# Performance work log

Measured on AMD Instinct MI355X. Metric: run time of the kernel, lower is better.

## Reference

```python
import jax, jax.numpy as jnp
import numpy as np

N = 50000
E = 800000
F_IN = 500
ID_DIM = 128
HID = 128
N_CLS = 40


def _init_linear(key, fan_in, fan_out, bias=True):
    k1, k2 = jax.random.split(key)
    bound = 1.0 / np.sqrt(fan_in)
    W = jax.random.uniform(k1, (fan_in, fan_out), minval=-bound, maxval=bound, dtype=jnp.float32)
    if bias:
        b = jax.random.uniform(k2, (fan_out,), minval=-bound, maxval=bound, dtype=jnp.float32)
        return W, b
    return W, None


def setup_inputs() -> dict:
    key = jax.random.key(0)
    ks = jax.random.split(key, 10)
    x = jax.random.normal(ks[0], (N, F_IN), dtype=jnp.float32)
    edge_index = jax.random.randint(ks[1], (2, E), 0, N, dtype=jnp.int32)
    W_map, b_map = _init_linear(ks[2], F_IN, ID_DIM)
    Wl1, bl1 = _init_linear(ks[3], ID_DIM, HID)
    Wr1, _ = _init_linear(ks[4], ID_DIM, HID, bias=False)
    Wl2, bl2 = _init_linear(ks[5], HID, 2 * HID)
    Wr2, _ = _init_linear(ks[6], HID, 2 * HID, bias=False)
    Wl3, bl3 = _init_linear(ks[7], 2 * HID, N_CLS)
    Wr3, _ = _init_linear(ks[8], 2 * HID, N_CLS, bias=False)
    return {"x": x, "edge_index": edge_index,
            "W_map": W_map, "b_map": b_map,
            "Wl1": Wl1, "bl1": bl1, "Wr1": Wr1,
            "Wl2": Wl2, "bl2": bl2, "Wr2": Wr2,
            "Wl3": Wl3, "bl3": bl3, "Wr3": Wr3}


def _sage_conv(x, src, dst, Wl, bl, Wr):
    # mean aggregation of source features into destination nodes
    agg = jax.ops.segment_sum(x[src], dst, num_segments=N)  # [N, d]
    cnt = jax.ops.segment_sum(jnp.ones((src.shape[0],), x.dtype), dst, num_segments=N)
    mean = agg / jnp.maximum(cnt, 1.0)[:, None]
    # SAGEConv (normalize=False): lin_l(mean_neigh) + lin_r(x), bias only on lin_l
    return mean @ Wl + bl + x @ Wr


def reference(x, edge_index, W_map, b_map, Wl1, bl1, Wr1, Wl2, bl2, Wr2, Wl3, bl3, Wr3):
    src, dst = edge_index[0], edge_index[1]
    h = x @ W_map + b_map                      # [N, 128]
    h = jax.nn.relu(_sage_conv(h, src, dst, Wl1, bl1, Wr1))   # dropout is identity in eval
    h = jax.nn.relu(_sage_conv(h, src, dst, Wl2, bl2, Wr2))
    h = _sage_conv(h, src, dst, Wl3, bl3, Wr3)
    return jax.nn.log_softmax(h, axis=1)
```

## Files before the change

kernel.cpp:

```cpp
#include <hip/hip_runtime.h>
#include <math.h>

#define NN 50000
#define NE 800000
#define FIN 500
#define NCLS 40
#define NB 196

typedef short short8 __attribute__((ext_vector_type(8)));
typedef float f32x4 __attribute__((ext_vector_type(4)));

__device__ __forceinline__ unsigned short f2bf(float f) {
    unsigned u = __float_as_uint(f);
    unsigned r = (u + 0x7FFFu + ((u >> 16) & 1u)) >> 16;
    return (unsigned short)r;
}
__device__ __forceinline__ float bf2f(unsigned short h) {
    return __uint_as_float(((unsigned)h) << 16);
}

typedef const __attribute__((address_space(1))) void gv1;
typedef __attribute__((address_space(3))) void lv3;
__device__ __forceinline__ void gl16(const void* g, void* l) {
    __builtin_amdgcn_global_load_lds((gv1*)g, (lv3*)l, 16, 0, 0);
}

__global__ void k_wsplit(const float* __restrict__ W, short* __restrict__ dst,
                         int Ksrc, int Ncols, int Kpad, int BN, int koff,
                         int noff, int llog) {
    int i = blockIdx.x * 256 + threadIdx.x;
    int len = 1 << llog;
    if (i >= Ncols * len) return;
    int n = i >> llog, kk = i & (len - 1);
    float v = (kk < Ksrc) ? W[(size_t)kk * Ncols + n] : 0.f;
    unsigned short hi = f2bf(v);
    float lo = v - bf2f(hi);
    int nd = noff + n, kd = koff + kk;
    int yb = nd / BN, r = nd % BN;
    int ck = kd >> 6, kin = kd & 63;
    int c16h = (kin >> 3) ^ (r & 7);
    size_t rowb = (((size_t)yb * (Kpad >> 6) + ck) * BN + r) * 128;
    dst[rowb + c16h * 8 + (kin & 7)] = (short)hi;
    dst[rowb + (8 + c16h) * 8 + (kin & 7)] = (short)f2bf(lo);
}

__global__ void k_count(const int* __restrict__ dst, int* __restrict__ deg) {
    int e = blockIdx.x * blockDim.x + threadIdx.x;
    if (e < NE) atomicAdd(&deg[dst[e]], 1);
}

__global__ void k_scan1(const int* __restrict__ deg, int* __restrict__ offs,
                        int* __restrict__ bsum) {
    __shared__ int sm[256];
    int tid = threadIdx.x;
    int i = blockIdx.x * 256 + tid;
    int v = (i < NN) ? deg[i] : 0;
    sm[tid] = v;
    __syncthreads();
    for (int off = 1; off < 256; off <<= 1) {
        int t = (tid >= off) ? sm[tid - off] : 0;
        __syncthreads();
        sm[tid] += t;
        __syncthreads();
    }
    if (i < NN) offs[i] = sm[tid] - v;
    if (tid == 255) bsum[blockIdx.x] = sm[255];
}

__global__ void k_scan2(const int* __restrict__ bsum, int* __restrict__ bpre,
                        int* __restrict__ offs) {
    __shared__ int sm[256];
    int tid = threadIdx.x;
    int v = (tid < NB) ? bsum[tid] : 0;
    sm[tid] = v;
    __syncthreads();
    for (int off = 1; off < 256; off <<= 1) {
        int t = (tid >= off) ? sm[tid - off] : 0;
        __syncthreads();
        sm[tid] += t;
        __syncthreads();
    }
    if (tid < NB) bpre[tid] = sm[tid] - v;
    if (tid == 255) offs[NN] = sm[255];
}

__global__ void k_scan3(int* __restrict__ offs, const int* __restrict__ bpre,
                        int* __restrict__ cursor) {
    int i = blockIdx.x * 256 + threadIdx.x;
    if (i < NN) {
        int v = offs[i] + bpre[blockIdx.x];
        offs[i] = v;
        cursor[i] = v;
    }
}

__global__ void k_scatter(const int* __restrict__ src, const int* __restrict__ dst,
                          int* __restrict__ cursor, int* __restrict__ ssrc) {
    int e = blockIdx.x * blockDim.x + threadIdx.x;
    if (e < NE) {
        int p = atomicAdd(&cursor[dst[e]], 1);
        ssrc[p] = src[e];
    }
}

__global__ __launch_bounds__(256) void k_aggb(
    const short* __restrict__ hb, const int* __restrict__ offs,
    const int* __restrict__ ssrc, short* __restrict__ mH) {
    int wid = (blockIdx.x * 256 + threadIdx.x) >> 6;
    int lane = threadIdx.x & 63;
    if (wid >= NN) return;
    int sub = lane >> 4, l16 = lane & 15;
    int beg = offs[wid], end = offs[wid + 1];
    f32x4 a0 = {0.f, 0.f, 0.f, 0.f}, a1 = {0.f, 0.f, 0.f, 0.f};
    int i = beg + sub;
    for (; i + 12 < end; i += 16) {
        int s0 = ssrc[i];
        int s1 = ssrc[i + 4];
        int s2 = ssrc[i + 8];
        int s3 = ssrc[i + 12];
        short8 v0 = *(const short8*)(hb + (size_t)s0 * 128 + l16 * 8);
        short8 v1 = *(const short8*)(hb + (size_t)s1 * 128 + l16 * 8);
        short8 v2 = *(const short8*)(hb + (size_t)s2 * 128 + l16 * 8);
        short8 v3 = *(const short8*)(hb + (size_t)s3 * 128 + l16 * 8);
#pragma unroll
        for (int j = 0; j < 4; ++j) {
            a0[j] += (bf2f((unsigned short)v0[j]) + bf2f((unsigned short)v1[j])) +
                     (bf2f((unsigned short)v2[j]) + bf2f((unsigned short)v3[j]));
            a1[j] += (bf2f((unsigned short)v0[j + 4]) + bf2f((unsigned short)v1[j + 4])) +
                     (bf2f((unsigned short)v2[j + 4]) + bf2f((unsigned short)v3[j + 4]));
        }
    }
    for (; i < end; i += 4) {
        int s0 = ssrc[i];
        short8 v0 = *(const short8*)(hb + (size_t)s0 * 128 + l16 * 8);
#pragma unroll
        for (int j = 0; j < 4; ++j) {
            a0[j] += bf2f((unsigned short)v0[j]);
            a1[j] += bf2f((unsigned short)v0[j + 4]);
        }
    }
#pragma unroll
    for (int j = 0; j < 4; ++j) {
        a0[j] += __shfl_xor(a0[j], 16);
        a0[j] += __shfl_xor(a0[j], 32);
        a1[j] += __shfl_xor(a1[j], 16);
        a1[j] += __shfl_xor(a1[j], 32);
    }
    if (sub == 0) {
        float inv = 1.f / fmaxf((float)(end - beg), 1.f);
        a0 *= inv; a1 *= inv;
        short8 hv;
#pragma unroll
        for (int j = 0; j < 4; ++j) {
            hv[j] = (short)f2bf(a0[j]);
            hv[j + 4] = (short)f2bf(a1[j]);
        }
        *(short8*)(mH + (size_t)wid * 128 + l16 * 8) = hv;
    }
}

template <int BN, int KPAD, int KS0, int KREAL, bool AFP32, bool RELU, bool PQ>
__global__ __launch_bounds__(512, 4) void k_mm5(
    const void* __restrict__ A0v, const short* __restrict__ A1,
    const short* __restrict__ Bg, const float* __restrict__ bias,
    short* __restrict__ CH, int ldc,
    float* __restrict__ F0, float* __restrict__ F1, int splitN,
    int M, int N) {
    constexpr int NT = BN / 16;
    constexpr int C = KPAD / 64;
    constexpr int PT = (BN * 16) / 512;
    constexpr int SLAB = BN * 128;
    static_assert((BN * 16) % 512 == 0, "staging divisibility");
    __shared__ short Bs[2 * SLAB];
    int tid = threadIdx.x;
    int wave = tid >> 6, lane = tid & 63;
    int quad = lane >> 4, l16 = lane & 15;
    int colBase = blockIdx.y * BN;
    int r0 = blockIdx.x * 128 + wave * 16 + l16;
    int r0c = min(r0, M - 1);
    const short* Bbase = Bg + (size_t)blockIdx.y * (C * SLAB);

    f32x4 acc[NT];
#pragma unroll
    for (int n = 0; n < NT; ++n) acc[n] = (f32x4){0.f, 0.f, 0.f, 0.f};

    auto stageB = [&](int buf, int ck) {
        const short* src = Bbase + (size_t)ck * SLAB;
        short* db = Bs + buf * SLAB;
#pragma unroll
        for (int u = 0; u < PT; ++u) {
            int base = u * 512 + wave * 64;
            gl16(src + (size_t)(base + lane) * 8, db + (size_t)base * 8);
        }
    };

    short8 aPre[AFP32 ? 2 : (2 * C)];
    short8 aCur[2];
    f32x4 fN[4];
    const float* Af = (const float*)A0v + (size_t)r0c * (size_t)KREAL;

    auto ldA32 = [&](int ck) {
#pragma unroll
        for (int s = 0; s < 2; ++s) {
            int kg = ck * 64 + s * 32 + quad * 8;
            f32x4 f0 = {0.f, 0.f, 0.f, 0.f}, f1 = {0.f, 0.f, 0.f, 0.f};
            if (kg < KREAL) f0 = *(const f32x4*)(Af + kg);
            if (kg + 4 < KREAL) f1 = *(const f32x4*)(Af + kg + 4);
            fN[s * 2] = f0;
            fN[s * 2 + 1] = f1;
        }
    };
    auto cvtA = [&]() {
#pragma unroll
        for (int s = 0; s < 2; ++s) {
            short8 a;
#pragma unroll
            for (int j = 0; j < 4; ++j) {
                a[j] = (short)f2bf(fN[s * 2][j]);
                a[j + 4] = (short)f2bf(fN[s * 2 + 1][j]);
            }
            aCur[s] = a;
        }
    };

    if constexpr (!AFP32) {
        const short* A0 = (const short*)A0v;
#pragma unroll
        for (int c = 0; c < C; ++c) {
            const bool seg = (c * 64 >= KS0);
            const short* ap = seg ? A1 : A0;
            const int w = seg ? (KPAD - KS0) : KS0;
            const int col = c * 64 - (seg ? KS0 : 0);
#pragma unroll
            for (int s = 0; s < 2; ++s)
                aPre[c * 2 + s] =
                    *(const short8*)(ap + (size_t)r0c * w + col + s * 32 + quad * 8);
        }
    } else {
        ldA32(0);
        cvtA();
    }

    stageB(0, 0);
    __syncthreads();

#pragma unroll
    for (int ck = 0; ck < C; ++ck) {
        if (ck + 1 < C) {
            stageB((ck + 1) & 1, ck + 1);
            if constexpr (AFP32) ldA32(ck + 1);
        }
        const short* bb = Bs + (ck & 1) * SLAB;
#pragma unroll
        for (int s = 0; s < 2; ++s) {
            short8 a;
            if constexpr (AFP32) a = aCur[s];
            else                 a = aPre[ck * 2 + s];
#pragma unroll
            for (int n = 0; n < NT; ++n) {
                int r = n * 16 + l16;
                int ch = (s * 4 + quad) ^ (r & 7);
                short8 bh = *(const short8*)(bb + r * 128 + ch * 8);
                short8 bl = *(const short8*)(bb + r * 128 + (8 + ch) * 8);
                acc[n] = __builtin_amdgcn_mfma_f32_16x16x32_bf16(a, bh, acc[n], 0, 0, 0);
                acc[n] = __builtin_amdgcn_mfma_f32_16x16x32_bf16(a, bl, acc[n], 0, 0, 0);
            }
        }
        if (ck + 1 < C) {
            __syncthreads();
            if constexpr (AFP32) cvtA();
        }
    }

    int gr0 = blockIdx.x * 128 + wave * 16 + quad * 4;
#pragma unroll
    for (int n = 0; n < NT; ++n) {
        int gc = colBase + n * 16 + l16;
        if (gc >= N) continue;
        float b = bias ? bias[gc] : 0.f;
#pragma unroll
        for (int r = 0; r < 4; ++r) {
            int gr = gr0 + r;
            if (gr < M) {
                float v = acc[n][r] + b;
                if (RELU) v = fmaxf(v, 0.f);
                if constexpr (PQ) {
                    if (gc < splitN) CH[(size_t)gr * ldc + gc] = (short)f2bf(v);
                    else             F0[(size_t)gr * (N - splitN) + (gc - splitN)] = v;
                } else {
                    if (CH) CH[(size_t)gr * ldc + gc] = (short)f2bf(v);
                    if (F0) {
                        if (gc < splitN) F0[(size_t)gr * splitN + gc] = v;
                        else             F1[(size_t)gr * (N - splitN) + (gc - splitN)] = v;
                    }
                }
            }
        }
    }
}

__global__ __launch_bounds__(256) void k_final(
    const short* __restrict__ pH, const float* __restrict__ q,
    const int* __restrict__ offs, const int* __restrict__ ssrc,
    const float* __restrict__ bl3, float* __restrict__ out) {
    int wid = (blockIdx.x * 256 + threadIdx.x) >> 6;
    int lane = threadIdx.x & 63;
    if (wid >= NN) return;
    bool act = lane < NCLS;
    int beg = offs[wid], end = offs[wid + 1];
    float a0 = 0.f, a1 = 0.f, a2 = 0.f, a3 = 0.f;
    int i = beg;
    for (; i + 3 < end; i += 4) {
        int s0 = ssrc[i], s1 = ssrc[i + 1], s2 = ssrc[i + 2], s3 = ssrc[i + 3];
        if (act) {
            a0 += bf2f((unsigned short)pH[(size_t)s0 * 64 + lane]);
            a1 += bf2f((unsigned short)pH[(size_t)s1 * 64 + lane]);
            a2 += bf2f((unsigned short)pH[(size_t)s2 * 64 + lane]);
            a3 += bf2f((unsigned short)pH[(size_t)s3 * 64 + lane]);
        }
    }
    for (; i < end; ++i) {
        int s0 = ssrc[i];
        if (act) a0 += bf2f((unsigned short)pH[(size_t)s0 * 64 + lane]);
    }
    float inv = 1.f / fmaxf((float)(end - beg), 1.f);
    float v = act ? ((a0 + a1) + (a2 + a3)) * inv + bl3[lane] + q[(size_t)wid * NCLS + lane]
                  : -INFINITY;
    float m = v;
#pragma unroll
    for (int off = 32; off > 0; off >>= 1) m = fmaxf(m, __shfl_xor(m, off));
    float e = act ? expf(v - m) : 0.f;
    float s = e;
#pragma unroll
    for (int off = 32; off > 0; off >>= 1) s += __shfl_xor(s, off);
    float ls = logf(s);
    if (act) out[(size_t)wid * NCLS + lane] = v - m - ls;
}

extern "C" void kernel_launch(void* const* d_in, const int* in_sizes, int n_in,
                              void* d_out, int out_size, void* d_ws, size_t ws_size,
                              hipStream_t stream) {
    const float* x    = (const float*)d_in[0];
    const int*   ei   = (const int*)d_in[1];
    const int*   esrc = ei;
    const int*   edst = ei + NE;
    const float* W_map = (const float*)d_in[2];
    const float* b_map = (const float*)d_in[3];
    const float* Wl1   = (const float*)d_in[4];
    const float* bl1   = (const float*)d_in[5];
    const float* Wr1   = (const float*)d_in[6];
    const float* Wl2   = (const float*)d_in[7];
    const float* bl2   = (const float*)d_in[8];
    const float* Wr2   = (const float*)d_in[9];
    const float* Wl3   = (const float*)d_in[10];
    const float* bl3   = (const float*)d_in[11];
    const float* Wr3   = (const float*)d_in[12];
    float* out = (float*)d_out;

    char* ws = (char*)d_ws;
    short* h0H = (short*)ws; ws += (size_t)NN * 128 * 2;
    short* m0H = (short*)ws; ws += (size_t)NN * 128 * 2;
    short* h1H = (short*)ws; ws += (size_t)NN * 128 * 2;
    short* m1H = (short*)ws; ws += (size_t)NN * 128 * 2;
    short* h2H = (short*)ws; ws += (size_t)NN * 256 * 2;
    short* pH  = (short*)ws; ws += (size_t)NN * 64 * 2;
    float* q   = (float*)ws; ws += (size_t)NN * NCLS * 4;
    short* wt  = (short*)ws; ws += (size_t)376832 * 2;
    int* deg    = (int*)ws;  ws += (size_t)NN * 4;
    int* offs   = (int*)ws;  ws += (size_t)(NN + 2) * 4;
    int* cursor = (int*)ws;  ws += (size_t)NN * 4;
    int* ssrc   = (int*)ws;  ws += (size_t)NE * 4;
    int* bsum   = (int*)ws;  ws += (size_t)256 * 4;
    int* bpre   = (int*)ws;  ws += (size_t)256 * 4;

    short* m_w  = wt + 0;
    short* b1w  = wt + 131072;
    short* b2w  = wt + 196608;
    short* b3w  = wt + 327680;

    (void)hipMemsetAsync(b3w, 0, (size_t)49152 * 2, stream);
    k_wsplit<<<(128 * 512 + 255) / 256, 256, 0, stream>>>(W_map, m_w, FIN, 128, 512, 128, 0, 0, 9);
    k_wsplit<<<(128 * 128 + 255) / 256, 256, 0, stream>>>(Wr1, b1w, 128, 128, 256, 128, 0, 0, 7);
    k_wsplit<<<(128 * 128 + 255) / 256, 256, 0, stream>>>(Wl1, b1w, 128, 128, 256, 128, 128, 0, 7);
    k_wsplit<<<(256 * 128 + 255) / 256, 256, 0, stream>>>(Wr2, b2w, 128, 256, 256, 128, 0, 0, 7);
    k_wsplit<<<(256 * 128 + 255) / 256, 256, 0, stream>>>(Wl2, b2w, 128, 256, 256, 128, 128, 0, 7);
    k_wsplit<<<(40 * 256 + 255) / 256, 256, 0, stream>>>(Wl3, b3w, 256, 40, 256, 96, 0, 0, 8);
    k_wsplit<<<(40 * 256 + 255) / 256, 256, 0, stream>>>(Wr3, b3w, 256, 40, 256, 96, 0, 40, 8);

    (void)hipMemsetAsync(deg, 0, (size_t)NN * 4, stream);
    k_count<<<(NE + 255) / 256, 256, 0, stream>>>(edst, deg);
    k_scan1<<<NB, 256, 0, stream>>>(deg, offs, bsum);
    k_scan2<<<1, 256, 0, stream>>>(bsum, bpre, offs);
    k_scan3<<<NB, 256, 0, stream>>>(offs, bpre, cursor);
    k_scatter<<<(NE + 255) / 256, 256, 0, stream>>>(esrc, edst, cursor, ssrc);

    const int g128 = (NN + 127) / 128;
    const int aggBlocks = (NN * 64) / 256;

    k_mm5<128, 512, 512, FIN, true, false, false><<<dim3(g128, 1), 512, 0, stream>>>(
        (const void*)x, nullptr, m_w, b_map,
        h0H, 128, nullptr, nullptr, 0, NN, 128);

    k_aggb<<<aggBlocks, 256, 0, stream>>>(h0H, offs, ssrc, m0H);

    k_mm5<128, 256, 128, 256, false, true, false><<<dim3(g128, 1), 512, 0, stream>>>(
        (const void*)h0H, m0H, b1w, bl1,
        h1H, 128, nullptr, nullptr, 0, NN, 128);

    k_aggb<<<aggBlocks, 256, 0, stream>>>(h1H, offs, ssrc, m1H);

    k_mm5<128, 256, 128, 256, false, true, false><<<dim3(g128, 2), 512, 0, stream>>>(
        (const void*)h1H, m1H, b2w, bl2,
        h2H, 256, nullptr, nullptr, 0, NN, 256);

    k_mm5<96, 256, 256, 256, false, false, true><<<dim3(g128, 1), 512, 0, stream>>>(
        (const void*)h2H, nullptr, b3w, nullptr,
        pH, 64, q, nullptr, NCLS, NN, 80);

    k_final<<<aggBlocks, 256, 0, stream>>>(pH, q, offs, ssrc, bl3, out);
}
```

Before: 467.2 us.

## Restructure GEMM main loop with one barrier per chunk and two-deep fp32 A prefetch

Rewrites the k_mm GEMM K-loop into a peeled pipeline. Each chunk now has a single barrier preceded by an explicit vmcnt wait, replacing the stage-then-sync pattern. The fp32 A operand (the x @ W_map layer) is double-buffered in registers and loaded two chunks ahead, so global loads overlap more MFMA work. This costs extra VGPRs for the second fp32 slot, relies on hand-counted vmcnt values, and adds sched_barriers that constrain compiler scheduling.

```diff
diff --git a/kernel.cpp b/kernel.cpp
--- a/kernel.cpp
+++ b/kernel.cpp
@@ -160,7 +160,7 @@
 }
 
 template <int BN, int KPAD, int KS0, int KREAL, bool AFP32, bool RELU, bool PQ>
-__global__ __launch_bounds__(512, 4) void k_mm5(
+__global__ __launch_bounds__(512, 4) void k_mm8(
     const void* __restrict__ A0v, const short* __restrict__ A1,
     const short* __restrict__ Bg, const float* __restrict__ bias,
     short* __restrict__ CH, int ldc,
@@ -170,7 +170,9 @@
     constexpr int C = KPAD / 64;
     constexpr int PT = (BN * 16) / 512;
     constexpr int SLAB = BN * 128;
+    constexpr int NA = AFP32 ? 4 : 0;
     static_assert((BN * 16) % 512 == 0, "staging divisibility");
+    static_assert(C >= 3, "peel structure needs >=3 chunks");
     __shared__ short Bs[2 * SLAB];
     int tid = threadIdx.x;
     int wave = tid >> 6, lane = tid & 63;
@@ -196,60 +198,33 @@
 
     short8 aPre[AFP32 ? 2 : (2 * C)];
     short8 aCur[2];
-    f32x4 fN[4];
+    f32x4 fN[2][4];
     const float* Af = (const float*)A0v + (size_t)r0c * (size_t)KREAL;
 
-    auto ldA32 = [&](int ck) {
+    auto ldA32 = [&](int slot, int ck) {
 #pragma unroll
         for (int s = 0; s < 2; ++s) {
             int kg = ck * 64 + s * 32 + quad * 8;
             f32x4 f0 = {0.f, 0.f, 0.f, 0.f}, f1 = {0.f, 0.f, 0.f, 0.f};
             if (kg < KREAL) f0 = *(const f32x4*)(Af + kg);
             if (kg + 4 < KREAL) f1 = *(const f32x4*)(Af + kg + 4);
-            fN[s * 2] = f0;
-            fN[s * 2 + 1] = f1;
+            fN[slot][s * 2] = f0;
+            fN[slot][s * 2 + 1] = f1;
         }
     };
-    auto cvtA = [&]() {
+    auto cvtA = [&](int slot) {
 #pragma unroll
         for (int s = 0; s < 2; ++s) {
             short8 a;
 #pragma unroll
             for (int j = 0; j < 4; ++j) {
-                a[j] = (short)f2bf(fN[s * 2][j]);
-                a[j + 4] = (short)f2bf(fN[s * 2 + 1][j]);
+                a[j] = (short)f2bf(fN[slot][s * 2][j]);
+                a[j + 4] = (short)f2bf(fN[slot][s * 2 + 1][j]);
             }
             aCur[s] = a;
         }
     };
-
-    if constexpr (!AFP32) {
-        const short* A0 = (const short*)A0v;
-#pragma unroll
-        for (int c = 0; c < C; ++c) {
-            const bool seg = (c * 64 >= KS0);
-            const short* ap = seg ? A1 : A0;
-            const int w = seg ? (KPAD - KS0) : KS0;
-            const int col = c * 64 - (seg ? KS0 : 0);
-#pragma unroll
-            for (int s = 0; s < 2; ++s)
-                aPre[c * 2 + s] =
-                    *(const short8*)(ap + (size_t)r0c * w + col + s * 32 + quad * 8);
-        }
-    } else {
-        ldA32(0);
-        cvtA();
-    }
-
-    stageB(0, 0);
-    __syncthreads();
-
-#pragma unroll
-    for (int ck = 0; ck < C; ++ck) {
-        if (ck + 1 < C) {
-            stageB((ck + 1) & 1, ck + 1);
-            if constexpr (AFP32) ldA32(ck + 1);
-        }
+    auto compute = [&](int ck) {
         const short* bb = Bs + (ck & 1) * SLAB;
 #pragma unroll
         for (int s = 0; s < 2; ++s) {
@@ -266,10 +241,43 @@
                 acc[n] = __builtin_amdgcn_mfma_f32_16x16x32_bf16(a, bl, acc[n], 0, 0, 0);
             }
         }
-        if (ck + 1 < C) {
-            __syncthreads();
-            if constexpr (AFP32) cvtA();
-        }
+    };
+
+    if constexpr (!AFP32) {
+        const short* A0 = (const short*)A0v;
+#pragma unroll
+        for (int c = 0; c < C; ++c) {
+            const bool seg = (c * 64 >= KS0);
+            const short* ap = seg ? A1 : A0;
+            const int w = seg ? (KPAD - KS0) : KS0;
+            const int col = c * 64 - (seg ? KS0 : 0);
+#pragma unroll
+            for (int s = 0; s < 2; ++s)
+                aPre[c * 2 + s] =
+                    *(const short8*)(ap + (size_t)r0c * w + col + s * 32 + quad * 8);
+        }
+    }
+    stageB(0, 0);
+    if constexpr (AFP32) { ldA32(0, 0); ldA32(1, 1); }
+
+#pragma unroll
+    for (int ck = 0; ck <= C - 2; ++ck) {
+        asm volatile("s_waitcnt vmcnt(%0)" ::"n"(NA) : "memory");
+        __builtin_amdgcn_s_barrier();
+        __builtin_amdgcn_sched_barrier(0);
+        stageB((ck + 1) & 1, ck + 1);
+        if constexpr (AFP32) {
+            cvtA(ck & 1);
+            if (ck + 2 < C) ldA32(ck & 1, ck + 2);
+        }
+        compute(ck);
+    }
+    {
+        asm volatile("s_waitcnt vmcnt(0)" ::: "memory");
+        __builtin_amdgcn_s_barrier();
+        __builtin_amdgcn_sched_barrier(0);
+        if constexpr (AFP32) cvtA((C - 1) & 1);
+        compute(C - 1);
     }
 
     int gr0 = blockIdx.x * 128 + wave * 16 + quad * 4;
@@ -397,23 +405,23 @@
     const int g128 = (NN + 127) / 128;
     const int aggBlocks = (NN * 64) / 256;
 
-    k_mm5<128, 512, 512, FIN, true, false, false><<<dim3(g128, 1), 512, 0, stream>>>(
+    k_mm8<128, 512, 512, FIN, true, false, false><<<dim3(g128, 1), 512, 0, stream>>>(
         (const void*)x, nullptr, m_w, b_map,
         h0H, 128, nullptr, nullptr, 0, NN, 128);
 
     k_aggb<<<aggBlocks, 256, 0, stream>>>(h0H, offs, ssrc, m0H);
 
-    k_mm5<128, 256, 128, 256, false, true, false><<<dim3(g128, 1), 512, 0, stream>>>(
+    k_mm8<128, 256, 128, 256, false, true, false><<<dim3(g128, 1), 512, 0, stream>>>(
         (const void*)h0H, m0H, b1w, bl1,
         h1H, 128, nullptr, nullptr, 0, NN, 128);
 
     k_aggb<<<aggBlocks, 256, 0, stream>>>(h1H, offs, ssrc, m1H);
 
-    k_mm5<128, 256, 128, 256, false, true, false><<<dim3(g128, 2), 512, 0, stream>>>(
+    k_mm8<128, 256, 128, 256, false, true, false><<<dim3(g128, 2), 512, 0, stream>>>(
         (const void*)h1H, m1H, b2w, bl2,
         h2H, 256, nullptr, nullptr, 0, NN, 256);
 
-    k_mm5<96, 256, 256, 256, false, false, true><<<dim3(g128, 1), 512, 0, stream>>>(
+    k_mm8<96, 256, 256, 256, false, false, true><<<dim3(g128, 1), 512, 0, stream>>>(
         (const void*)h2H, nullptr, b3w, nullptr,
         pH, 64, q, nullptr, NCLS, NN, 80);
 
```

Measured after the change: 462.1 us. About the same (-1.1%).
